# Kernel optimization log

Measured on AMD Instinct MI355X. Metric: run time of the kernel, lower is better.

The kernel has to match this reference:

```python
import jax, jax.numpy as jnp
import numpy as np

C, W = 144, 9225          # channel_count, batch_width
KW, F = 10, 64            # kernel_width, fc_segment_length
H1 = 128                  # second layer out
CAT = 2 * C * F           # 18432 = C*F (fc) + (W-KW+1) (conv)


def setup_inputs() -> dict:
    key = jax.random.key(0)
    ks = jax.random.split(key, 9)
    s_fc = 1.0 / np.sqrt(W)
    s_cv = 1.0 / np.sqrt(C * KW)
    s_1 = 1.0 / np.sqrt(CAT)
    s_2 = 1.0 / np.sqrt(H1)
    return {
        "x":     jax.random.normal(ks[0], (C, W), jnp.float32),
        "Wfc":   jax.random.normal(ks[1], (C, F, W), jnp.float32) * s_fc,
        "bfc":   jax.random.normal(ks[2], (C, F), jnp.float32) * s_fc,
        "Kconv": jax.random.normal(ks[3], (C, KW), jnp.float32) * s_cv,
        "bconv": jax.random.normal(ks[4], (1,), jnp.float32) * s_cv,
        "W1":    jax.random.normal(ks[5], (H1, CAT), jnp.float32) * s_1,
        "b1":    jax.random.normal(ks[6], (H1,), jnp.float32) * s_1,
        "W2":    jax.random.normal(ks[7], (1, H1), jnp.float32) * s_2,
        "b2":    jax.random.normal(ks[8], (1,), jnp.float32) * s_2,
    }


def reference(x, Wfc, bfc, Kconv, bconv, W1, b1, W2, b2):
    # 144 per-channel Linear(W->F) fused into one batched GEMV (no ReLU on
    # these in the original forward, despite the docstring).
    fc_out = (jnp.einsum('cfw,cw->cf', Wfc, x) + bfc).reshape(-1)  # [C*F]
    # Conv2d(1,1,(C,KW)): kernel height == channel count -> 1D valid corr.
    conv = jax.lax.conv_general_dilated(
        x[None, None],            # [1,1,C,W]
        Kconv[None, None],        # [1,1,C,KW]
        window_strides=(1, 1), padding='VALID')[0, 0, 0] + bconv  # [W-KW+1]
    concatenated = jnp.concatenate([fc_out, conv])                # [CAT]
    second = jax.nn.relu(W1 @ concatenated + b1)                  # [H1]
    out = jax.nn.relu(W2 @ second + b2)                           # [1]
    return jax.nn.sigmoid(out)
```

## Files before the change

kernel.cpp:

```cpp
#include <hip/hip_runtime.h>
#include <math.h>

#define CC    144
#define WW    9225
#define KWW   10
#define FF    64
#define H1N   128
#define CONVN (WW - KWW + 1)
#define CFN   (CC * FF)
#define CATN  (CFN + CONVN)
#define FCB   (CFN / 4)
#define NFULL 144
#define NTAIL 9

typedef float f32x4 __attribute__((ext_vector_type(4)));

__global__ __launch_bounds__(256) void k_front_v5(
    const float* __restrict__ x,
    const float* __restrict__ Wfc,
    const float* __restrict__ bfc,
    const float* __restrict__ Kc,
    const float* __restrict__ bconv,
    float* __restrict__ concat)
{
    __shared__ float sm[CC * KWW];
    const int bid = blockIdx.x;
    const int tid = threadIdx.x;

    if (bid < FCB) {
        const int wave = tid >> 6;
        const int lane = tid & 63;
        const int r    = bid * 4 + wave;
        const int c    = r >> 6;
        const float* __restrict__ wr = Wfc + (size_t)r * WW;
        const float* __restrict__ xr = x + (size_t)c * WW;

        const float* __restrict__ wp = wr + lane;
        const float* __restrict__ xp = xr + lane;

        float acc = 0.f;
        #pragma unroll 8
        for (int k = 0; k < NFULL; ++k)
            acc = fmaf(wp[(size_t)k * 64], xp[(size_t)k * 64], acc);
        if (lane < NTAIL)
            acc += wr[NFULL * 64 + lane] * xr[NFULL * 64 + lane];

        #pragma unroll
        for (int off = 32; off > 0; off >>= 1)
            acc += __shfl_xor(acc, off, 64);
        if (lane == 0)
            concat[r] = acc + bfc[r];
    } else {
        for (int i = tid; i < CC * KWW; i += 256) sm[i] = Kc[i];
        __syncthreads();

        const int p = (bid - FCB) * 256 + tid;
        float acc = bconv[0];
        for (int c = 0; c < CC; ++c) {
            const float* __restrict__ xr = x + (size_t)c * WW + p;
            const float* __restrict__ kr = sm + c * KWW;
            #pragma unroll
            for (int k = 0; k < KWW; ++k)
                acc = fmaf(xr[k], kr[k], acc);
        }
        concat[CFN + p] = acc;
    }
}

__global__ __launch_bounds__(256) void k_layer1_v2(
    const float* __restrict__ W1,
    const float* __restrict__ concat,
    float* __restrict__ partial)
{
    __shared__ float sm[4];
    const int j = blockIdx.x, tid = threadIdx.x;
    const int h = j >> 1, half = j & 1;
    const f32x4* __restrict__ wr =
        (const f32x4*)(W1 + (size_t)h * CATN + half * (CATN / 2));
    const f32x4* __restrict__ cv =
        (const f32x4*)(concat + half * (CATN / 2));

    float acc = 0.f;
    for (int i = tid; i < CATN / 8; i += 256) {
        const f32x4 a = wr[i];
        const f32x4 q = cv[i];
        acc += a.x * q.x + a.y * q.y + a.z * q.z + a.w * q.w;
    }
    #pragma unroll
    for (int off = 32; off > 0; off >>= 1)
        acc += __shfl_xor(acc, off, 64);
    if ((tid & 63) == 0) sm[tid >> 6] = acc;
    __syncthreads();
    if (tid == 0)
        partial[j] = sm[0] + sm[1] + sm[2] + sm[3];
}

__global__ __launch_bounds__(128) void k_final_v2(
    const float* __restrict__ partial,
    const float* __restrict__ b1,
    const float* __restrict__ W2,
    const float* __restrict__ b2,
    float* __restrict__ out)
{
    __shared__ float sm[2];
    const int tid = threadIdx.x;
    float v = fmaxf(partial[2 * tid] + partial[2 * tid + 1] + b1[tid], 0.f)
              * W2[tid];
    #pragma unroll
    for (int off = 32; off > 0; off >>= 1)
        v += __shfl_xor(v, off, 64);
    if ((tid & 63) == 0) sm[tid >> 6] = v;
    __syncthreads();
    if (tid == 0) {
        float z = sm[0] + sm[1] + b2[0];
        z = fmaxf(z, 0.f);
        out[0] = 1.f / (1.f + expf(-z));
    }
}

extern "C" void kernel_launch(void* const* d_in, const int* in_sizes, int n_in,
                              void* d_out, int out_size, void* d_ws, size_t ws_size,
                              hipStream_t stream) {
    const float* x     = (const float*)d_in[0];
    const float* Wfc   = (const float*)d_in[1];
    const float* bfc   = (const float*)d_in[2];
    const float* Kc    = (const float*)d_in[3];
    const float* bconv = (const float*)d_in[4];
    const float* W1    = (const float*)d_in[5];
    const float* b1    = (const float*)d_in[6];
    const float* W2    = (const float*)d_in[7];
    const float* b2    = (const float*)d_in[8];
    float* out = (float*)d_out;

    float* concat  = (float*)d_ws;
    float* partial = concat + CATN;

    k_front_v5 <<<FCB + (CONVN / 256), 256, 0, stream>>>(
        x, Wfc, bfc, Kc, bconv, concat);
    k_layer1_v2<<<256, 256, 0, stream>>>(W1, concat, partial);
    k_final_v2 <<<1, 128, 0, stream>>>(partial, b1, W2, b2, out);
}
```

Baseline: 88.93 us.

## Stage x row in shared memory and compute two FC rows per wave

The FC path now assigns 8 blocks per channel. Each block copies that channel's x row (9225 floats) into LDS, then each wave computes two Wfc output rows that share the cached x value. This cuts redundant global reads of x and halves the block count for the FC part. In exchange it costs a large LDS allocation (about 36KB per block), which may reduce occupancy for both FC and conv blocks, plus an added barrier and load phase.

```diff
diff --git a/kernel.cpp b/kernel.cpp
--- a/kernel.cpp
+++ b/kernel.cpp
@@ -9,13 +9,13 @@
 #define CONVN (WW - KWW + 1)
 #define CFN   (CC * FF)
 #define CATN  (CFN + CONVN)
-#define FCB   (CFN / 4)
+#define FCB2  (CC * 8)
 #define NFULL 144
 #define NTAIL 9
 
 typedef float f32x4 __attribute__((ext_vector_type(4)));
 
-__global__ __launch_bounds__(256) void k_front_v5(
+__global__ __launch_bounds__(256) void k_front_v6(
     const float* __restrict__ x,
     const float* __restrict__ Wfc,
     const float* __restrict__ bfc,
@@ -23,42 +23,58 @@
     const float* __restrict__ bconv,
     float* __restrict__ concat)
 {
-    __shared__ float sm[CC * KWW];
+    __shared__ float smem[WW];
     const int bid = blockIdx.x;
     const int tid = threadIdx.x;
 
-    if (bid < FCB) {
+    if (bid < FCB2) {
+        const int c = bid >> 3;
+        const int g = bid & 7;
+        const float* __restrict__ xr = x + (size_t)c * WW;
+
+        for (int i = tid; i < WW; i += 256) smem[i] = xr[i];
+        __syncthreads();
+
         const int wave = tid >> 6;
         const int lane = tid & 63;
-        const int r    = bid * 4 + wave;
-        const int c    = r >> 6;
-        const float* __restrict__ wr = Wfc + (size_t)r * WW;
-        const float* __restrict__ xr = x + (size_t)c * WW;
+        const int f0   = g * 8 + wave * 2;
+        const int r0   = (c << 6) + f0;
+        const float* __restrict__ w0 = Wfc + (size_t)r0 * WW + lane;
+        const float* __restrict__ w1 = w0 + WW;
 
-        const float* __restrict__ wp = wr + lane;
-        const float* __restrict__ xp = xr + lane;
-
-        float acc = 0.f;
+        float a0 = 0.f, a1 = 0.f;
         #pragma unroll 8
-        for (int k = 0; k < NFULL; ++k)
-            acc = fmaf(wp[(size_t)k * 64], xp[(size_t)k * 64], acc);
-        if (lane < NTAIL)
-            acc += wr[NFULL * 64 + lane] * xr[NFULL * 64 + lane];
+        for (int k = 0; k < NFULL; ++k) {
+            const int idx = (k << 6);
+            const float xv = smem[idx + lane];
+            a0 = fmaf(w0[idx], xv, a0);
+            a1 = fmaf(w1[idx], xv, a1);
+        }
+        if (lane < NTAIL) {
+            const int idx = NFULL * 64 + lane;
+            const float xv = smem[idx];
+            a0 = fmaf(w0[idx - lane + lane], xv, a0);
+            a1 = fmaf(w1[idx - lane + lane], xv, a1);
+        }
 
         #pragma unroll
-        for (int off = 32; off > 0; off >>= 1)
-            acc += __shfl_xor(acc, off, 64);
-        if (lane == 0)
-            concat[r] = acc + bfc[r];
+        for (int off = 32; off > 0; off >>= 1) {
+            a0 += __shfl_xor(a0, off, 64);
+            a1 += __shfl_xor(a1, off, 64);
+        }
+        if (lane == 0) {
+            concat[r0]     = a0 + bfc[r0];
+            concat[r0 + 1] = a1 + bfc[r0 + 1];
+        }
     } else {
-        for (int i = tid; i < CC * KWW; i += 256) sm[i] = Kc[i];
+        for (int i = tid; i < CC * KWW; i += 256) smem[i] = Kc[i];
         __syncthreads();
 
-        const int p = (bid - FCB) * 256 + tid;
+        const int p = (bid - FCB2) * 256 + tid;
         float acc = bconv[0];
         for (int c = 0; c < CC; ++c) {
             const float* __restrict__ xr = x + (size_t)c * WW + p;
-            const float* __restrict__ kr = sm + c * KWW;
+            const float* __restrict__ kr = smem + c * KWW;
             #pragma unroll
             for (int k = 0; k < KWW; ++k)
                 acc = fmaf(xr[k], kr[k], acc);
@@ -135,7 +151,7 @@
     float* concat  = (float*)d_ws;
     float* partial = concat + CATN;
 
-    k_front_v5 <<<FCB + (CONVN / 256), 256, 0, stream>>>(
+    k_front_v6 <<<FCB2 + (CONVN / 256), 256, 0, stream>>>(
         x, Wfc, bfc, Kc, bconv, concat);
     k_layer1_v2<<<256, 256, 0, stream>>>(W1, concat, partial);
     k_final_v2 <<<1, 128, 0, stream>>>(partial, b1, W2, b2, out);
```

Result: no change. 88.84 us (-0.1%).

## Stream Wfc as flat vectorized grid-stride sweep with atomic row accumulation

Applied to the files above, without the earlier changes.

Replaces the one-wave-per-row FC GEMV with a persistent grid-stride sweep over the flattened Wfc tensor. Each thread reads 8 contiguous floats with nontemporal vector loads, does a wave reduction and issues an atomicAdd into the output row, handling waves that straddle two rows. Bias initialization moves to a separate init kernel. The goal is fully coalesced 32-byte-per-lane streaming of the roughly 340MB weight tensor. In exchange it adds an extra launch, per-iteration atomics and unaligned x loads.

```diff
diff --git a/kernel.cpp b/kernel.cpp
--- a/kernel.cpp
+++ b/kernel.cpp
@@ -9,61 +9,99 @@
 #define CONVN (WW - KWW + 1)
 #define CFN   (CC * FF)
 #define CATN  (CFN + CONVN)
-#define FCB   (CFN / 4)
-#define NFULL 144
-#define NTAIL 9
+#define CONVB 36
+#define SWEEPB 2048
+#define GRIDTH (SWEEPB * 256)
+#define NQ8   (CC * FF * WW / 8)
+#define ADVF  (GRIDTH * 8)
+#define DR    (ADVF / WW)
+#define RREM  (ADVF % WW)
+#define L1B   256
 
-typedef float f32x4 __attribute__((ext_vector_type(4)));
+typedef float f32x4  __attribute__((ext_vector_type(4)));
+typedef float f32x4u __attribute__((ext_vector_type(4), aligned(4)));
 
-__global__ __launch_bounds__(256) void k_front_v5(
+__global__ __launch_bounds__(256) void k_init(
+    const float* __restrict__ bfc, float* __restrict__ concat)
+{
+    const int i = blockIdx.x * 256 + threadIdx.x;
+    if (i < CFN) concat[i] = bfc[i];
+}
+
+__global__ __launch_bounds__(256) void k_sweep(
     const float* __restrict__ x,
     const float* __restrict__ Wfc,
-    const float* __restrict__ bfc,
     const float* __restrict__ Kc,
     const float* __restrict__ bconv,
     float* __restrict__ concat)
 {
-    __shared__ float sm[CC * KWW];
+    __shared__ float kc[CC * KWW];
     const int bid = blockIdx.x;
     const int tid = threadIdx.x;
 
-    if (bid < FCB) {
-        const int wave = tid >> 6;
-        const int lane = tid & 63;
-        const int r    = bid * 4 + wave;
-        const int c    = r >> 6;
-        const float* __restrict__ wr = Wfc + (size_t)r * WW;
-        const float* __restrict__ xr = x + (size_t)c * WW;
-
-        const float* __restrict__ wp = wr + lane;
-        const float* __restrict__ xp = xr + lane;
-
-        float acc = 0.f;
-        #pragma unroll 8
-        for (int k = 0; k < NFULL; ++k)
-            acc = fmaf(wp[(size_t)k * 64], xp[(size_t)k * 64], acc);
-        if (lane < NTAIL)
-            acc += wr[NFULL * 64 + lane] * xr[NFULL * 64 + lane];
-
-        #pragma unroll
-        for (int off = 32; off > 0; off >>= 1)
-            acc += __shfl_xor(acc, off, 64);
-        if (lane == 0)
-            concat[r] = acc + bfc[r];
-    } else {
-        for (int i = tid; i < CC * KWW; i += 256) sm[i] = Kc[i];
+    if (bid < CONVB) {
+        for (int i = tid; i < CC * KWW; i += 256) kc[i] = Kc[i];
         __syncthreads();
-
-        const int p = (bid - FCB) * 256 + tid;
+        const int p = bid * 256 + tid;
         float acc = bconv[0];
-        for (int c = 0; c < CC; ++c) {
-            const float* __restrict__ xr = x + (size_t)c * WW + p;
-            const float* __restrict__ kr = sm + c * KWW;
+        for (int c2 = 0; c2 < CC; ++c2) {
+            const float* __restrict__ xr = x + (size_t)c2 * WW + p;
+            const float* __restrict__ kr = kc + c2 * KWW;
             #pragma unroll
             for (int k = 0; k < KWW; ++k)
                 acc = fmaf(xr[k], kr[k], acc);
         }
         concat[CFN + p] = acc;
+        return;
+    }
+
+    const int gid  = (bid - CONVB) * 256 + tid;
+    const int lane = tid & 63;
+    unsigned flat = (unsigned)gid * 8u;
+    int r   = (int)(flat / WW);
+    int off = (int)(flat % WW);
+
+    for (unsigned j = (unsigned)gid; j < (unsigned)NQ8; j += (unsigned)GRIDTH) {
+        const float* __restrict__ wp = Wfc + (size_t)j * 8u;
+        const f32x4 w0 = __builtin_nontemporal_load((const f32x4*)wp);
+        const f32x4 w1 = __builtin_nontemporal_load((const f32x4*)wp + 1);
+
+        float pa = 0.f, pb = 0.f;
+        const int c = r >> 6;
+        if (off <= WW - 8) {
+            const f32x4u* __restrict__ xp =
+                (const f32x4u*)(x + (size_t)c * WW + off);
+            const f32x4 x0 = xp[0], x1 = xp[1];
+            pa = w0.x * x0.x + w0.y * x0.y + w0.z * x0.z + w0.w * x0.w
+               + w1.x * x1.x + w1.y * x1.y + w1.z * x1.z + w1.w * x1.w;
+        } else {
+            const float wv[8] = {w0.x, w0.y, w0.z, w0.w, w1.x, w1.y, w1.z, w1.w};
+            const int c2 = (r + 1) >> 6;
+            #pragma unroll
+            for (int k = 0; k < 8; ++k) {
+                const int e = off + k;
+                if (e < WW) pa = fmaf(wv[k], x[(size_t)c  * WW + e],        pa);
+                else        pb = fmaf(wv[k], x[(size_t)c2 * WW + (e - WW)], pb);
+            }
+        }
+
+        const int r0 = __builtin_amdgcn_readfirstlane(r);
+        float ga = (r == r0) ? pa : 0.f;
+        float gb = (r == r0) ? pb : pa;
+        const int cross = __any(gb != 0.f);
+        #pragma unroll
+        for (int o = 32; o; o >>= 1) ga += __shfl_xor(ga, o, 64);
+        if (cross) {
+            #pragma unroll
+            for (int o = 32; o; o >>= 1) gb += __shfl_xor(gb, o, 64);
+        }
+        if (lane == 0) {
+            atomicAdd(&concat[r0], ga);
+            if (cross) atomicAdd(&concat[r0 + 1], gb);
+        }
+
+        off += RREM; r += DR;
+        if (off >= WW) { off -= WW; ++r; }
     }
 }
 
@@ -135,8 +173,8 @@
     float* concat  = (float*)d_ws;
     float* partial = concat + CATN;
 
-    k_front_v5 <<<FCB + (CONVN / 256), 256, 0, stream>>>(
-        x, Wfc, bfc, Kc, bconv, concat);
-    k_layer1_v2<<<256, 256, 0, stream>>>(W1, concat, partial);
-    k_final_v2 <<<1, 128, 0, stream>>>(partial, b1, W2, b2, out);
+    k_init     <<<(CFN + 255) / 256, 256, 0, stream>>>(bfc, concat);
+    k_sweep    <<<CONVB + SWEEPB,    256, 0, stream>>>(x, Wfc, Kc, bconv, concat);
+    k_layer1_v2<<<L1B,               256, 0, stream>>>(W1, concat, partial);
+    k_final_v2 <<<1,                 128, 0, stream>>>(partial, b1, W2, b2, out);
 }
```

Measured after the change: 125.8 us. +41.5%, slower.
